# Kernel tuning notes

Hardware: AMD Instinct MI355X
Metric: run time of the kernel (lower is better)

Reference implementation:

```python
import jax, jax.numpy as jnp
import numpy as np

B, C_IN, C_OUT, N, K = 4, 64, 64, 100000, 6
EPS = 1e-5  # BatchNorm2d default eps


def setup_inputs() -> dict:
    key = jax.random.key(0)
    k1, k2, k3, k4 = jax.random.split(key, 4)
    x = jax.random.normal(k1, (B, C_IN, N), jnp.float32)
    neigh = jax.random.randint(k2, (B, N, K), 0, N, jnp.int32)
    # bias-free 1x2 conv weights (center feature + neighbor-sum symmetric operator)
    W0 = jax.random.normal(k3, (C_OUT, C_IN, 2), jnp.float32) * (1.0 / np.sqrt(C_IN * 2))
    W1 = jax.random.normal(k4, (C_OUT, C_OUT, 2), jnp.float32) * (1.0 / np.sqrt(C_OUT * 2))
    gamma = jnp.ones((C_OUT,), jnp.float32)
    beta = jnp.zeros((C_OUT,), jnp.float32)
    return {"x": x, "neigh": neigh, "W0": W0, "W1": W1, "gamma": gamma, "beta": beta}


def _mesh_conv_point(x, neigh, W):
    # x: [B, C, N], neigh: [B, N, K] -> gather neighbor features [B, C, N, K]
    nb = jax.vmap(lambda xb, ib: xb[:, ib])(x, neigh)
    # symmetric operator stack: center feature and sum over neighbors -> [B, C, N, 2]
    G = jnp.stack([x, nb.sum(axis=-1)], axis=-1)
    # 1x2 conv (bias=False) as einsum -> [B, O, N]
    return jnp.einsum('bcns,ocs->bon', G, W)


def _batchnorm(h, gamma, beta):
    # training-mode batch stats over (batch, vertex) per channel
    mean = h.mean(axis=(0, 2), keepdims=True)
    var = h.var(axis=(0, 2), keepdims=True)
    return (h - mean) * jax.lax.rsqrt(var + EPS) * gamma[None, :, None] + beta[None, :, None]


def reference(x, neigh, W0, W1, gamma, beta):
    h = _mesh_conv_point(x, neigh, W0)
    x1 = h  # residual branch
    h = _batchnorm(jax.nn.relu(h), gamma, beta)
    h = _mesh_conv_point(h, neigh, W1)
    h = h + x1
    return jax.nn.relu(h)
```

## Files before the change

kernel.cpp:

```cpp
#include <hip/hip_runtime.h>
#include <hip/hip_bf16.h>

#define BB   4
#define NN   100000
#define TOT  (BB * NN)
#define KK   6
#define EPSV 1e-5f

using bf16   = __hip_bfloat16;
using ushort = unsigned short;
typedef __attribute__((ext_vector_type(8))) short  short8;
typedef __attribute__((ext_vector_type(4))) float  float4v;

union U4S8 { uint4 u; short8 s; };

__device__ __forceinline__ unsigned f2bu(float f) {
    union { bf16 h; ushort u; } c; c.h = __float2bfloat16(f); return c.u;
}
__device__ __forceinline__ unsigned pk(float a, float b) {
    return f2bu(a) | (f2bu(b) << 16);
}
__device__ __forceinline__ float blo(unsigned x) {
    union { unsigned u; float f; } c; c.u = x << 16; return c.f;
}
__device__ __forceinline__ float bhi(unsigned x) {
    union { unsigned u; float f; } c; c.u = x & 0xFFFF0000u; return c.f;
}
__device__ __forceinline__ unsigned relu2(unsigned x) {
    unsigned lo = (unsigned)(((int)(x << 16)) >> 31) & 0x0000FFFFu;
    unsigned hi = ((unsigned)(((int)x) >> 31)) << 16;
    return x & ~(lo | hi);
}
__device__ __forceinline__ int batch_base(int g) {
    return (g >= 3 * NN) ? 3 * NN : (g >= 2 * NN) ? 2 * NN : (g >= NN) ? NN : 0;
}

__device__ __forceinline__ void gload_lds16(const void* g, void* l)
{
    __builtin_amdgcn_global_load_lds(
        (const __attribute__((address_space(1))) unsigned int*)g,
        (__attribute__((address_space(3))) unsigned int*)l, 16, 0, 0);
}

__global__ void wprep0_k(const float* __restrict__ W0, ushort* __restrict__ Wf0)
{
    int L = blockIdx.x * 256 + threadIdx.x;
    if (L < 8192) {
        int i = L & 7, lane = (L >> 3) & 63, r = L >> 9;
        int s = r & 1, t = r >> 1;
        int o = (t & 3) * 16 + (lane & 15);
        int c = s * 32 + (lane >> 4) * 8 + i;
        Wf0[L] = f2bu(W0[o * 128 + c * 2 + (t >> 2)]);
    }
}

__global__ __launch_bounds__(256) void xpose_k(const float* __restrict__ x,
                                               ushort* __restrict__ xT)
{
    __shared__ float tile[64][65];
    const int b  = blockIdx.y;
    const int n0 = blockIdx.x * 64;
    const int tx = threadIdx.x & 63;
    const int ty = threadIdx.x >> 6;
    const float* xb = x + (size_t)b * 64 * NN;
    const int n = n0 + tx;
#pragma unroll
    for (int cc = 0; cc < 64; cc += 4) {
        const int c = cc + ty;
        tile[tx][c] = (n < NN) ? xb[(size_t)c * NN + n] : 0.f;
    }
    __syncthreads();
#pragma unroll
    for (int rr = 0; rr < 64; rr += 4) {
        const int nl = rr + ty;
        const int n2 = n0 + nl;
        if (n2 < NN) xT[((size_t)b * NN + n2) * 64 + tx] = (ushort)f2bu(tile[nl][tx]);
    }
}

__global__ __launch_bounds__(256, 3) void gemm1_k(
    const ushort* __restrict__ xT, const ushort* __restrict__ Wf,
    ushort* __restrict__ Uu, ushort* __restrict__ Uv)
{
    const int wave = threadIdx.x >> 6;
    const int lane = threadIdx.x & 63;
    const int col  = lane & 15;
    const int quad = lane >> 4;

    short8 wf[8][2];
#pragma unroll
    for (int t = 0; t < 8; ++t)
#pragma unroll
        for (int s = 0; s < 2; ++s)
            wf[t][s] = *(const short8*)(Wf + ((t * 2 + s) * 64 + lane) * 8);

    const int wid = blockIdx.x * 4 + wave;
    for (int tile = wid; tile < 25000; tile += 2500) {
        const size_t g0 = (size_t)tile * 16;
        const ushort* ar = xT + (g0 + col) * 64 + quad * 8;
        short8 p0 = *(const short8*)(ar);
        short8 p1 = *(const short8*)(ar + 32);

        float4v acc[8];
#pragma unroll
        for (int t = 0; t < 8; ++t) acc[t] = (float4v){0.f, 0.f, 0.f, 0.f};
#pragma unroll
        for (int t = 0; t < 8; ++t)
            acc[t] = __builtin_amdgcn_mfma_f32_16x16x32_bf16(wf[t][0], p0, acc[t], 0, 0, 0);
#pragma unroll
        for (int t = 0; t < 8; ++t)
            acc[t] = __builtin_amdgcn_mfma_f32_16x16x32_bf16(wf[t][1], p1, acc[t], 0, 0, 0);

#pragma unroll
        for (int t = 0; t < 8; ++t) {
            uint2 d;
            d.x = pk(acc[t][0], acc[t][1]);
            d.y = pk(acc[t][2], acc[t][3]);
            ushort* base = (t < 4) ? Uu : Uv;
            *(uint2*)(base + (g0 + col) * 64 + (t & 3) * 16 + quad * 4) = d;
        }
    }
}

__global__ __launch_bounds__(256, 3) void gather1_k(
    const ushort* __restrict__ Uu, const ushort* __restrict__ Uv,
    const int* __restrict__ neigh, ushort* __restrict__ hT,
    float* __restrict__ stats)
{
    __shared__ __align__(1024) ushort stage[4][3072];
    __shared__ float red[4][128];
    const int wave = threadIdx.x >> 6;
    const int lane = threadIdx.x & 63;
    const int p    = lane >> 3;
    const int s    = lane & 7;
    const int g0   = (blockIdx.x * 4 + wave) * 32;

    ushort* stg = stage[wave];
    const int csw = ((s - p) & 7) * 8;
    const int rsw = ((s + p) & 7) * 8;
    const uint2* nbp = (const uint2*)neigh;

    float sA[8] = {0,0,0,0,0,0,0,0}, sB[8] = {0,0,0,0,0,0,0,0};

    for (int t = 0; t < 4; ++t) {
        const int gme = g0 + t * 8 + p;
        const int bo  = batch_base(gme);

        uint2 i01 = nbp[(size_t)gme * 3 + 0];
        uint2 i23 = nbp[(size_t)gme * 3 + 1];
        uint2 i45 = nbp[(size_t)gme * 3 + 2];
        int idx[6] = {(int)i01.x, (int)i01.y, (int)i23.x,
                      (int)i23.y, (int)i45.x, (int)i45.y};

        uint4 cu = *(const uint4*)(Uu + (size_t)gme * 64 + s * 8);

#pragma unroll
        for (int m = 0; m < 6; ++m)
            gload_lds16(Uv + (size_t)(bo + idx[m]) * 64 + csw, stg + m * 512);

        asm volatile("s_waitcnt vmcnt(0)" ::: "memory");

        float h[8];
        h[0] = blo(cu.x); h[1] = bhi(cu.x); h[2] = blo(cu.y); h[3] = bhi(cu.y);
        h[4] = blo(cu.z); h[5] = bhi(cu.z); h[6] = blo(cu.w); h[7] = bhi(cu.w);
#pragma unroll
        for (int m = 0; m < 6; ++m) {
            const uint4 r = *(const uint4*)(stg + m * 512 + p * 64 + rsw);
            h[0] += blo(r.x); h[1] += bhi(r.x); h[2] += blo(r.y); h[3] += bhi(r.y);
            h[4] += blo(r.z); h[5] += bhi(r.z); h[6] += blo(r.w); h[7] += bhi(r.w);
        }
        uint4 st;
        st.x = pk(h[0], h[1]); st.y = pk(h[2], h[3]);
        st.z = pk(h[4], h[5]); st.w = pk(h[6], h[7]);
        *(uint4*)(hT + (size_t)gme * 64 + s * 8) = st;
#pragma unroll
        for (int j = 0; j < 8; ++j) {
            float rv = fmaxf(h[j], 0.f);
            sA[j] += rv;
            sB[j]  = fmaf(rv, rv, sB[j]);
        }
    }

#pragma unroll
    for (int d = 8; d < 64; d <<= 1)
#pragma unroll
        for (int j = 0; j < 8; ++j) {
            sA[j] += __shfl_xor(sA[j], d);
            sB[j] += __shfl_xor(sB[j], d);
        }
    if (lane < 8) {
#pragma unroll
        for (int j = 0; j < 8; ++j) {
            red[wave][lane * 8 + j]      = sA[j];
            red[wave][64 + lane * 8 + j] = sB[j];
        }
    }
    __syncthreads();
    if (threadIdx.x < 128) {
        float v = red[0][threadIdx.x] + red[1][threadIdx.x]
                + red[2][threadIdx.x] + red[3][threadIdx.x];
        atomicAdd(&stats[threadIdx.x], v);
    }
}

__global__ void bnA_k(const float* __restrict__ stats, const float* __restrict__ gamma,
                      const float* __restrict__ beta, float* __restrict__ ab)
{
    const int o = threadIdx.x;
    if (o < 64) {
        const float inv = 1.f / (float)TOT;
        float mean = stats[o] * inv;
        float var  = stats[64 + o] * inv - mean * mean;
        float a    = gamma[o] * rsqrtf(var + EPSV);
        ab[o]      = a;
        ab[64 + o] = fmaf(-a, mean, beta[o]);
    }
}

__global__ __launch_bounds__(256) void bnB_k(
    const float* __restrict__ ab, const float* __restrict__ W1,
    ushort* __restrict__ Wf1, float* __restrict__ bias)
{
    if (blockIdx.x < 32) {
        int L = blockIdx.x * 256 + threadIdx.x;
        int i = L & 7, lane = (L >> 3) & 63, r = L >> 9;
        int s = r & 1, t = r >> 1;
        int o = (t & 3) * 16 + (lane & 15);
        int c = s * 32 + (lane >> 4) * 8 + i;
        Wf1[L] = f2bu(ab[c] * W1[o * 128 + c * 2 + (t >> 2)]);
    } else if (threadIdx.x < 128) {
        const int part = threadIdx.x >> 6, o = threadIdx.x & 63;
        float s = 0.f;
#pragma unroll
        for (int c = 0; c < 64; ++c)
            s = fmaf(ab[64 + c], W1[o * 128 + c * 2 + part], s);
        bias[threadIdx.x] = s;
    }
}

__global__ __launch_bounds__(256, 3) void gemm2_k(
    const ushort* __restrict__ hT, const ushort* __restrict__ Wf,
    const float* __restrict__ bias, ushort* __restrict__ Up,
    ushort* __restrict__ Uq)
{
    const int wave = threadIdx.x >> 6;
    const int lane = threadIdx.x & 63;
    const int col  = lane & 15;
    const int quad = lane >> 4;

    short8 wf[8][2];
#pragma unroll
    for (int t = 0; t < 8; ++t)
#pragma unroll
        for (int s = 0; s < 2; ++s)
            wf[t][s] = *(const short8*)(Wf + ((t * 2 + s) * 64 + lane) * 8);

    float4v binit[8];
#pragma unroll
    for (int t = 0; t < 8; ++t)
#pragma unroll
        for (int r = 0; r < 4; ++r)
            binit[t][r] = bias[t * 16 + quad * 4 + r];

    const int wid = blockIdx.x * 4 + wave;
    for (int tile = wid; tile < 25000; tile += 2500) {
        const size_t g0 = (size_t)tile * 16;
        const ushort* ar = hT + (g0 + col) * 64 + quad * 8;
        U4S8 p0, p1;
        p0.u = *(const uint4*)(ar);
        p1.u = *(const uint4*)(ar + 32);
        p0.u.x = relu2(p0.u.x); p0.u.y = relu2(p0.u.y);
        p0.u.z = relu2(p0.u.z); p0.u.w = relu2(p0.u.w);
        p1.u.x = relu2(p1.u.x); p1.u.y = relu2(p1.u.y);
        p1.u.z = relu2(p1.u.z); p1.u.w = relu2(p1.u.w);

        float4v acc[8];
#pragma unroll
        for (int t = 0; t < 8; ++t) acc[t] = binit[t];
#pragma unroll
        for (int t = 0; t < 8; ++t)
            acc[t] = __builtin_amdgcn_mfma_f32_16x16x32_bf16(wf[t][0], p0.s, acc[t], 0, 0, 0);
#pragma unroll
        for (int t = 0; t < 8; ++t)
            acc[t] = __builtin_amdgcn_mfma_f32_16x16x32_bf16(wf[t][1], p1.s, acc[t], 0, 0, 0);

#pragma unroll
        for (int t = 0; t < 8; ++t) {
            uint2 d;
            d.x = pk(acc[t][0], acc[t][1]);
            d.y = pk(acc[t][2], acc[t][3]);
            ushort* base = (t < 4) ? Up : Uq;
            *(uint2*)(base + (g0 + col) * 64 + (t & 3) * 16 + quad * 4) = d;
        }
    }
}

__global__ __launch_bounds__(256, 3) void gather2_k(
    const ushort* __restrict__ Up, const ushort* __restrict__ Uq,
    const ushort* __restrict__ hT, const int* __restrict__ neigh,
    float* __restrict__ out)
{
    __shared__ __align__(1024) ushort stage[4][3072];
    __shared__ float ts[64][65];
    const int wave = threadIdx.x >> 6;
    const int lane = threadIdx.x & 63;
    const int p    = lane >> 3;
    const int s    = lane & 7;
    const int g0   = blockIdx.x * 64;
    const int gw   = g0 + wave * 16;

    ushort* stg = stage[wave];
    const int csw = ((s - p) & 7) * 8;
    const int rsw = ((s + p) & 7) * 8;
    const uint2* nbp = (const uint2*)neigh;

#pragma unroll
    for (int t = 0; t < 2; ++t) {
        const int gme = gw + t * 8 + p;
        const int bo  = batch_base(gme);

        uint2 i01 = nbp[(size_t)gme * 3 + 0];
        uint2 i23 = nbp[(size_t)gme * 3 + 1];
        uint2 i45 = nbp[(size_t)gme * 3 + 2];
        int idx[6] = {(int)i01.x, (int)i01.y, (int)i23.x,
                      (int)i23.y, (int)i45.x, (int)i45.y};

        uint4 cp = *(const uint4*)(Up + (size_t)gme * 64 + s * 8);
        uint4 cr = *(const uint4*)(hT + (size_t)gme * 64 + s * 8);

#pragma unroll
        for (int m = 0; m < 6; ++m)
            gload_lds16(Uq + (size_t)(bo + idx[m]) * 64 + csw, stg + m * 512);

        asm volatile("s_waitcnt vmcnt(0)" ::: "memory");

        float h[8];
        h[0] = blo(cp.x) + blo(cr.x); h[1] = bhi(cp.x) + bhi(cr.x);
        h[2] = blo(cp.y) + blo(cr.y); h[3] = bhi(cp.y) + bhi(cr.y);
        h[4] = blo(cp.z) + blo(cr.z); h[5] = bhi(cp.z) + bhi(cr.z);
        h[6] = blo(cp.w) + blo(cr.w); h[7] = bhi(cp.w) + bhi(cr.w);
#pragma unroll
        for (int m = 0; m < 6; ++m) {
            const uint4 r = *(const uint4*)(stg + m * 512 + p * 64 + rsw);
            h[0] += blo(r.x); h[1] += bhi(r.x); h[2] += blo(r.y); h[3] += bhi(r.y);
            h[4] += blo(r.z); h[5] += bhi(r.z); h[6] += blo(r.w); h[7] += bhi(r.w);
        }
        const int pl = wave * 16 + t * 8 + p;
#pragma unroll
        for (int j = 0; j < 8; ++j)
            ts[s * 8 + j][pl] = fmaxf(h[j], 0.f);
    }
    __syncthreads();

    const int g2  = g0 + lane;
    const int bo2 = batch_base(g2);
    const int b2  = (g2 >= 3 * NN) ? 3 : (g2 >= 2 * NN) ? 2 : (g2 >= NN) ? 1 : 0;
    const int n2  = g2 - bo2;
#pragma unroll
    for (int r = 0; r < 16; ++r) {
        const int o = wave * 16 + r;
        out[((size_t)b2 * 64 + o) * NN + n2] = ts[o][lane];
    }
}

extern "C" void kernel_launch(void* const* d_in, const int* in_sizes, int n_in,
                              void* d_out, int out_size, void* d_ws, size_t ws_size,
                              hipStream_t stream)
{
    const float* x     = (const float*)d_in[0];
    const int*   neigh = (const int*)d_in[1];
    const float* W0    = (const float*)d_in[2];
    const float* W1    = (const float*)d_in[3];
    const float* gamma = (const float*)d_in[4];
    const float* beta  = (const float*)d_in[5];
    float* out = (float*)d_out;

    char* ws = (char*)d_ws;
    ushort* xT    = (ushort*)(ws + 0);
    ushort* hT    = (ushort*)(ws + 0);
    ushort* Uu    = (ushort*)(ws + 51200000);
    ushort* Uv    = (ushort*)(ws + 102400000);
    ushort* Up    = Uu;
    ushort* Uq    = Uv;
    float*  stats = (float*)(ws + 153600000);
    float*  ab    = (float*)(ws + 153600512);
    ushort* Wf0   = (ushort*)(ws + 153601024);
    ushort* Wf1   = (ushort*)(ws + 153617408);
    float*  bias  = (float*)(ws + 153633792);

    hipMemsetAsync(stats, 0, 512, stream);
    wprep0_k<<<dim3(32), dim3(256), 0, stream>>>(W0, Wf0);
    xpose_k<<<dim3((NN + 63) / 64, BB), dim3(256), 0, stream>>>(x, xT);
    gemm1_k<<<dim3(625), dim3(256), 0, stream>>>(xT, Wf0, Uu, Uv);
    gather1_k<<<dim3(3125), dim3(256), 0, stream>>>(Uu, Uv, neigh, hT, stats);
    bnA_k<<<dim3(1), dim3(64), 0, stream>>>(stats, gamma, beta, ab);
    bnB_k<<<dim3(33), dim3(256), 0, stream>>>(ab, W1, Wf1, bias);
    gemm2_k<<<dim3(625), dim3(256), 0, stream>>>(hT, Wf1, bias, Up, Uq);
    gather2_k<<<dim3(TOT / 64), dim3(256), 0, stream>>>(Up, Uq, hT, neigh, out);
}
```

Baseline: 442.9 us.

## Split channel-major intermediates into 16-channel planes for cache-friendly neighbor gathers

Intermediate bf16 tensors are stored as four 16-channel planes of size TOT*16 instead of 64 contiguous channels per vertex. Each gather wave then handles a single plane, so the random neighbor reads for a pass touch a 12.8MB working set that may fit better in cache. The LDS staging via global_load_lds is replaced with direct uint4 register loads, and grids grow to 12500 blocks with higher occupancy bounds. The trade-off is that neighbor indices are reloaded four times, and each gathered row is now a smaller 32-byte segment.

```diff
diff --git a/kernel.cpp b/kernel.cpp
--- a/kernel.cpp
+++ b/kernel.cpp
@@ -31,16 +31,8 @@
     unsigned hi = ((unsigned)(((int)x) >> 31)) << 16;
     return x & ~(lo | hi);
 }
-__device__ __forceinline__ int batch_base(int g) {
-    return (g >= 3 * NN) ? 3 * NN : (g >= 2 * NN) ? 2 * NN : (g >= NN) ? NN : 0;
-}
-
-__device__ __forceinline__ void gload_lds16(const void* g, void* l)
-{
-    __builtin_amdgcn_global_load_lds(
-        (const __attribute__((address_space(1))) unsigned int*)g,
-        (__attribute__((address_space(3))) unsigned int*)l, 16, 0, 0);
-}
+
+#define PST ((size_t)TOT * 16)
 
 __global__ void wprep0_k(const float* __restrict__ W0, ushort* __restrict__ Wf0)
 {
@@ -117,89 +109,84 @@
             d.x = pk(acc[t][0], acc[t][1]);
             d.y = pk(acc[t][2], acc[t][3]);
             ushort* base = (t < 4) ? Uu : Uv;
-            *(uint2*)(base + (g0 + col) * 64 + (t & 3) * 16 + quad * 4) = d;
+            *(uint2*)(base + ((size_t)(t & 3) * TOT + g0 + col) * 16 + quad * 4) = d;
         }
     }
 }
 
-__global__ __launch_bounds__(256, 3) void gather1_k(
+__global__ __launch_bounds__(256, 6) void gather1_k(
     const ushort* __restrict__ Uu, const ushort* __restrict__ Uv,
     const int* __restrict__ neigh, ushort* __restrict__ hT,
     float* __restrict__ stats)
 {
-    __shared__ __align__(1024) ushort stage[4][3072];
-    __shared__ float red[4][128];
+    __shared__ float red[4][32];
     const int wave = threadIdx.x >> 6;
     const int lane = threadIdx.x & 63;
-    const int p    = lane >> 3;
-    const int s    = lane & 7;
-    const int g0   = (blockIdx.x * 4 + wave) * 32;
-
-    ushort* stg = stage[wave];
-    const int csw = ((s - p) & 7) * 8;
-    const int rsw = ((s + p) & 7) * 8;
-    const uint2* nbp = (const uint2*)neigh;
-
-    float sA[8] = {0,0,0,0,0,0,0,0}, sB[8] = {0,0,0,0,0,0,0,0};
-
-    for (int t = 0; t < 4; ++t) {
-        const int gme = g0 + t * 8 + p;
-        const int bo  = batch_base(gme);
-
-        uint2 i01 = nbp[(size_t)gme * 3 + 0];
-        uint2 i23 = nbp[(size_t)gme * 3 + 1];
-        uint2 i45 = nbp[(size_t)gme * 3 + 2];
-        int idx[6] = {(int)i01.x, (int)i01.y, (int)i23.x,
-                      (int)i23.y, (int)i45.x, (int)i45.y};
-
-        uint4 cu = *(const uint4*)(Uu + (size_t)gme * 64 + s * 8);
-
-#pragma unroll
-        for (int m = 0; m < 6; ++m)
-            gload_lds16(Uv + (size_t)(bo + idx[m]) * 64 + csw, stg + m * 512);
-
-        asm volatile("s_waitcnt vmcnt(0)" ::: "memory");
-
-        float h[8];
-        h[0] = blo(cu.x); h[1] = bhi(cu.x); h[2] = blo(cu.y); h[3] = bhi(cu.y);
-        h[4] = blo(cu.z); h[5] = bhi(cu.z); h[6] = blo(cu.w); h[7] = bhi(cu.w);
-#pragma unroll
-        for (int m = 0; m < 6; ++m) {
-            const uint4 r = *(const uint4*)(stg + m * 512 + p * 64 + rsw);
-            h[0] += blo(r.x); h[1] += bhi(r.x); h[2] += blo(r.y); h[3] += bhi(r.y);
-            h[4] += blo(r.z); h[5] += bhi(r.z); h[6] += blo(r.w); h[7] += bhi(r.w);
-        }
-        uint4 st;
-        st.x = pk(h[0], h[1]); st.y = pk(h[2], h[3]);
-        st.z = pk(h[4], h[5]); st.w = pk(h[6], h[7]);
-        *(uint4*)(hT + (size_t)gme * 64 + s * 8) = st;
-#pragma unroll
-        for (int j = 0; j < 8; ++j) {
-            float rv = fmaxf(h[j], 0.f);
-            sA[j] += rv;
-            sB[j]  = fmaf(rv, rv, sB[j]);
-        }
-    }
-
-#pragma unroll
-    for (int d = 8; d < 64; d <<= 1)
+    const int p    = lane >> 1;
+    const int e    = lane & 1;
+    const int wid  = blockIdx.x * 4 + wave;
+    const int q    = wid / 12500;
+    const int r    = wid - q * 12500;
+    const int b    = r / 3125;
+    const int grp  = r - b * 3125;
+    const int gme  = b * NN + grp * 32 + p;
+    const int bo   = b * NN;
+    const int eo   = e * 8;
+
+    const int* np = neigh + (size_t)gme * 6;
+    const uint2 i01 = *(const uint2*)(np);
+    const uint2 i23 = *(const uint2*)(np + 2);
+    const uint2 i45 = *(const uint2*)(np + 4);
+
+    const ushort* uvb = Uv + q * PST;
+    uint4 v0 = *(const uint4*)(uvb + ((size_t)(bo + (int)i01.x)) * 16 + eo);
+    uint4 v1 = *(const uint4*)(uvb + ((size_t)(bo + (int)i01.y)) * 16 + eo);
+    uint4 v2 = *(const uint4*)(uvb + ((size_t)(bo + (int)i23.x)) * 16 + eo);
+    uint4 v3 = *(const uint4*)(uvb + ((size_t)(bo + (int)i23.y)) * 16 + eo);
+    uint4 v4 = *(const uint4*)(uvb + ((size_t)(bo + (int)i45.x)) * 16 + eo);
+    uint4 v5 = *(const uint4*)(uvb + ((size_t)(bo + (int)i45.y)) * 16 + eo);
+    uint4 cu = *(const uint4*)(Uu + q * PST + (size_t)gme * 16 + eo);
+
+    float h[8];
+    h[0] = blo(cu.x); h[1] = bhi(cu.x); h[2] = blo(cu.y); h[3] = bhi(cu.y);
+    h[4] = blo(cu.z); h[5] = bhi(cu.z); h[6] = blo(cu.w); h[7] = bhi(cu.w);
+#define ACC8(v) { h[0]+=blo(v.x); h[1]+=bhi(v.x); h[2]+=blo(v.y); h[3]+=bhi(v.y); \
+                  h[4]+=blo(v.z); h[5]+=bhi(v.z); h[6]+=blo(v.w); h[7]+=bhi(v.w); }
+    ACC8(v0) ACC8(v1) ACC8(v2) ACC8(v3) ACC8(v4) ACC8(v5)
+
+    uint4 st;
+    st.x = pk(h[0], h[1]); st.y = pk(h[2], h[3]);
+    st.z = pk(h[4], h[5]); st.w = pk(h[6], h[7]);
+    *(uint4*)(hT + q * PST + (size_t)gme * 16 + eo) = st;
+
+    float sA[8], sB[8];
+#pragma unroll
+    for (int j = 0; j < 8; ++j) {
+        float rv = fmaxf(h[j], 0.f);
+        sA[j] = rv;
+        sB[j] = rv * rv;
+    }
+#pragma unroll
+    for (int d = 2; d < 64; d <<= 1)
 #pragma unroll
         for (int j = 0; j < 8; ++j) {
             sA[j] += __shfl_xor(sA[j], d);
             sB[j] += __shfl_xor(sB[j], d);
         }
-    if (lane < 8) {
+    if (lane < 2) {
 #pragma unroll
         for (int j = 0; j < 8; ++j) {
             red[wave][lane * 8 + j]      = sA[j];
-            red[wave][64 + lane * 8 + j] = sB[j];
+            red[wave][16 + lane * 8 + j] = sB[j];
         }
     }
     __syncthreads();
-    if (threadIdx.x < 128) {
+    if (threadIdx.x < 32) {
+        const int q0 = blockIdx.x / 3125;
         float v = red[0][threadIdx.x] + red[1][threadIdx.x]
                 + red[2][threadIdx.x] + red[3][threadIdx.x];
-        atomicAdd(&stats[threadIdx.x], v);
+        const int c = threadIdx.x & 15;
+        atomicAdd(&stats[(threadIdx.x < 16 ? 0 : 64) + q0 * 16 + c], v);
     }
 }
 
@@ -265,10 +252,10 @@
     const int wid = blockIdx.x * 4 + wave;
     for (int tile = wid; tile < 25000; tile += 2500) {
         const size_t g0 = (size_t)tile * 16;
-        const ushort* ar = hT + (g0 + col) * 64 + quad * 8;
+        const ushort* ar = hT + ((size_t)(quad >> 1) * TOT + g0 + col) * 16 + (quad & 1) * 8;
         U4S8 p0, p1;
         p0.u = *(const uint4*)(ar);
-        p1.u = *(const uint4*)(ar + 32);
+        p1.u = *(const uint4*)(ar + 2 * PST);
         p0.u.x = relu2(p0.u.x); p0.u.y = relu2(p0.u.y);
         p0.u.z = relu2(p0.u.z); p0.u.w = relu2(p0.u.w);
         p1.u.x = relu2(p1.u.x); p1.u.y = relu2(p1.u.y);
@@ -290,77 +277,55 @@
             d.x = pk(acc[t][0], acc[t][1]);
             d.y = pk(acc[t][2], acc[t][3]);
             ushort* base = (t < 4) ? Up : Uq;
-            *(uint2*)(base + (g0 + col) * 64 + (t & 3) * 16 + quad * 4) = d;
+            *(uint2*)(base + ((size_t)(t & 3) * TOT + g0 + col) * 16 + quad * 4) = d;
         }
     }
 }
 
-__global__ __launch_bounds__(256, 3) void gather2_k(
+__global__ __launch_bounds__(256, 6) void gather2_k(
     const ushort* __restrict__ Up, const ushort* __restrict__ Uq,
     const ushort* __restrict__ hT, const int* __restrict__ neigh,
     float* __restrict__ out)
 {
-    __shared__ __align__(1024) ushort stage[4][3072];
-    __shared__ float ts[64][65];
     const int wave = threadIdx.x >> 6;
     const int lane = threadIdx.x & 63;
-    const int p    = lane >> 3;
-    const int s    = lane & 7;
-    const int g0   = blockIdx.x * 64;
-    const int gw   = g0 + wave * 16;
-
-    ushort* stg = stage[wave];
-    const int csw = ((s - p) & 7) * 8;
-    const int rsw = ((s + p) & 7) * 8;
-    const uint2* nbp = (const uint2*)neigh;
-
-#pragma unroll
-    for (int t = 0; t < 2; ++t) {
-        const int gme = gw + t * 8 + p;
-        const int bo  = batch_base(gme);
-
-        uint2 i01 = nbp[(size_t)gme * 3 + 0];
-        uint2 i23 = nbp[(size_t)gme * 3 + 1];
-        uint2 i45 = nbp[(size_t)gme * 3 + 2];
-        int idx[6] = {(int)i01.x, (int)i01.y, (int)i23.x,
-                      (int)i23.y, (int)i45.x, (int)i45.y};
-
-        uint4 cp = *(const uint4*)(Up + (size_t)gme * 64 + s * 8);
-        uint4 cr = *(const uint4*)(hT + (size_t)gme * 64 + s * 8);
-
-#pragma unroll
-        for (int m = 0; m < 6; ++m)
-            gload_lds16(Uq + (size_t)(bo + idx[m]) * 64 + csw, stg + m * 512);
-
-        asm volatile("s_waitcnt vmcnt(0)" ::: "memory");
-
-        float h[8];
-        h[0] = blo(cp.x) + blo(cr.x); h[1] = bhi(cp.x) + bhi(cr.x);
-        h[2] = blo(cp.y) + blo(cr.y); h[3] = bhi(cp.y) + bhi(cr.y);
-        h[4] = blo(cp.z) + blo(cr.z); h[5] = bhi(cp.z) + bhi(cr.z);
-        h[6] = blo(cp.w) + blo(cr.w); h[7] = bhi(cp.w) + bhi(cr.w);
-#pragma unroll
-        for (int m = 0; m < 6; ++m) {
-            const uint4 r = *(const uint4*)(stg + m * 512 + p * 64 + rsw);
-            h[0] += blo(r.x); h[1] += bhi(r.x); h[2] += blo(r.y); h[3] += bhi(r.y);
-            h[4] += blo(r.z); h[5] += bhi(r.z); h[6] += blo(r.w); h[7] += bhi(r.w);
-        }
-        const int pl = wave * 16 + t * 8 + p;
-#pragma unroll
-        for (int j = 0; j < 8; ++j)
-            ts[s * 8 + j][pl] = fmaxf(h[j], 0.f);
-    }
-    __syncthreads();
-
-    const int g2  = g0 + lane;
-    const int bo2 = batch_base(g2);
-    const int b2  = (g2 >= 3 * NN) ? 3 : (g2 >= 2 * NN) ? 2 : (g2 >= NN) ? 1 : 0;
-    const int n2  = g2 - bo2;
-#pragma unroll
-    for (int r = 0; r < 16; ++r) {
-        const int o = wave * 16 + r;
-        out[((size_t)b2 * 64 + o) * NN + n2] = ts[o][lane];
-    }
+    const int p    = lane >> 1;
+    const int e    = lane & 1;
+    const int wid  = blockIdx.x * 4 + wave;
+    const int q    = wid / 12500;
+    const int r    = wid - q * 12500;
+    const int b    = r / 3125;
+    const int grp  = r - b * 3125;
+    const int gme  = b * NN + grp * 32 + p;
+    const int bo   = b * NN;
+    const int eo   = e * 8;
+
+    const int* np = neigh + (size_t)gme * 6;
+    const uint2 i01 = *(const uint2*)(np);
+    const uint2 i23 = *(const uint2*)(np + 2);
+    const uint2 i45 = *(const uint2*)(np + 4);
+
+    const ushort* uqb = Uq + q * PST;
+    uint4 v0 = *(const uint4*)(uqb + ((size_t)(bo + (int)i01.x)) * 16 + eo);
+    uint4 v1 = *(const uint4*)(uqb + ((size_t)(bo + (int)i01.y)) * 16 + eo);
+    uint4 v2 = *(const uint4*)(uqb + ((size_t)(bo + (int)i23.x)) * 16 + eo);
+    uint4 v3 = *(const uint4*)(uqb + ((size_t)(bo + (int)i23.y)) * 16 + eo);
+    uint4 v4 = *(const uint4*)(uqb + ((size_t)(bo + (int)i45.x)) * 16 + eo);
+    uint4 v5 = *(const uint4*)(uqb + ((size_t)(bo + (int)i45.y)) * 16 + eo);
+    uint4 cp = *(const uint4*)(Up + q * PST + (size_t)gme * 16 + eo);
+    uint4 cr = *(const uint4*)(hT + q * PST + (size_t)gme * 16 + eo);
+
+    float h[8];
+    h[0] = blo(cp.x) + blo(cr.x); h[1] = bhi(cp.x) + bhi(cr.x);
+    h[2] = blo(cp.y) + blo(cr.y); h[3] = bhi(cp.y) + bhi(cr.y);
+    h[4] = blo(cp.z) + blo(cr.z); h[5] = bhi(cp.z) + bhi(cr.z);
+    h[6] = blo(cp.w) + blo(cr.w); h[7] = bhi(cp.w) + bhi(cr.w);
+    ACC8(v0) ACC8(v1) ACC8(v2) ACC8(v3) ACC8(v4) ACC8(v5)
+
+    float* ob = out + ((size_t)(b * 64 + q * 16 + e * 8)) * NN + grp * 32 + p;
+#pragma unroll
+    for (int j = 0; j < 8; ++j)
+        ob[(size_t)j * NN] = fmaxf(h[j], 0.f);
 }
 
 extern "C" void kernel_launch(void* const* d_in, const int* in_sizes, int n_in,
@@ -392,9 +357,9 @@
     wprep0_k<<<dim3(32), dim3(256), 0, stream>>>(W0, Wf0);
     xpose_k<<<dim3((NN + 63) / 64, BB), dim3(256), 0, stream>>>(x, xT);
     gemm1_k<<<dim3(625), dim3(256), 0, stream>>>(xT, Wf0, Uu, Uv);
-    gather1_k<<<dim3(3125), dim3(256), 0, stream>>>(Uu, Uv, neigh, hT, stats);
+    gather1_k<<<dim3(12500), dim3(256), 0, stream>>>(Uu, Uv, neigh, hT, stats);
     bnA_k<<<dim3(1), dim3(64), 0, stream>>>(stats, gamma, beta, ab);
     bnB_k<<<dim3(33), dim3(256), 0, stream>>>(ab, W1, Wf1, bias);
     gemm2_k<<<dim3(625), dim3(256), 0, stream>>>(hT, Wf1, bias, Up, Uq);
-    gather2_k<<<dim3(TOT / 64), dim3(256), 0, stream>>>(Up, Uq, hT, neigh, out);
-}
+    gather2_k<<<dim3(12500), dim3(256), 0, stream>>>(Up, Uq, hT, neigh, out);
+}
```

After: 476.5 us. 7.6% more time.

## Gather neighbor features before the GEMM and fuse the output transpose into gemm2

Applied to the files above, without the earlier changes.

Each mesh-conv stage now sums the 64-channel input features over the neighbors first (gatherx/gatherh), then runs a single K=128 MFMA GEMM over [center, neighbor-sum]. Before, the GEMM produced two 64-channel projections and the neighbor gather ran on the projected outputs. The reordering is meant to cut intermediate global-memory traffic: one sum buffer replaces the two projected buffers. BN statistics move into gemm1, and BN's shift is folded into the bias as 6x the neighbor weight. gemm2 now adds the residual and applies ReLU, then transposes through shared memory straight to the output, which removes the separate gather2 pass and its LDS-staged async loads. The risk is the extra gather passes, whose random 16-byte loads now go through plain vector loads.

```diff
diff --git a/kernel.cpp b/kernel.cpp
--- a/kernel.cpp
+++ b/kernel.cpp
@@ -35,22 +35,21 @@
     return (g >= 3 * NN) ? 3 * NN : (g >= 2 * NN) ? 2 * NN : (g >= NN) ? NN : 0;
 }
 
-__device__ __forceinline__ void gload_lds16(const void* g, void* l)
-{
-    __builtin_amdgcn_global_load_lds(
-        (const __attribute__((address_space(1))) unsigned int*)g,
-        (__attribute__((address_space(3))) unsigned int*)l, 16, 0, 0);
-}
+#define ACC8(v)  { h[0]+=blo(v.x); h[1]+=bhi(v.x); h[2]+=blo(v.y); h[3]+=bhi(v.y); \
+                   h[4]+=blo(v.z); h[5]+=bhi(v.z); h[6]+=blo(v.w); h[7]+=bhi(v.w); }
+#define ACCR8(v) { unsigned a0=relu2(v.x),a1=relu2(v.y),a2=relu2(v.z),a3=relu2(v.w); \
+                   h[0]+=blo(a0); h[1]+=bhi(a0); h[2]+=blo(a1); h[3]+=bhi(a1); \
+                   h[4]+=blo(a2); h[5]+=bhi(a2); h[6]+=blo(a3); h[7]+=bhi(a3); }
 
 __global__ void wprep0_k(const float* __restrict__ W0, ushort* __restrict__ Wf0)
 {
     int L = blockIdx.x * 256 + threadIdx.x;
     if (L < 8192) {
         int i = L & 7, lane = (L >> 3) & 63, r = L >> 9;
-        int s = r & 1, t = r >> 1;
-        int o = (t & 3) * 16 + (lane & 15);
-        int c = s * 32 + (lane >> 4) * 8 + i;
-        Wf0[L] = f2bu(W0[o * 128 + c * 2 + (t >> 2)]);
+        int t = r >> 2, ks = r & 3;
+        int o = t * 16 + (lane & 15);
+        int c = ks * 32 + (lane >> 4) * 8 + i;
+        Wf0[L] = f2bu(W0[o * 128 + (c & 63) * 2 + (c >> 6)]);
     }
 }
 
@@ -78,122 +77,122 @@
     }
 }
 
+__global__ __launch_bounds__(256, 4) void gatherx_k(
+    const ushort* __restrict__ xT, const int* __restrict__ neigh,
+    ushort* __restrict__ SX)
+{
+    const int wave = threadIdx.x >> 6;
+    const int lane = threadIdx.x & 63;
+    const int p    = lane >> 3;
+    const int s    = lane & 7;
+    const int so   = s * 8;
+    const int g0   = (blockIdx.x * 4 + wave) * 32;
+
+#pragma unroll
+    for (int t = 0; t < 4; ++t) {
+        const int gme = g0 + t * 8 + p;
+        const int bo  = batch_base(gme);
+        const int* np = neigh + (size_t)gme * 6;
+        const uint2 i01 = *(const uint2*)(np);
+        const uint2 i23 = *(const uint2*)(np + 2);
+        const uint2 i45 = *(const uint2*)(np + 4);
+
+        uint4 v0 = *(const uint4*)(xT + (size_t)(bo + (int)i01.x) * 64 + so);
+        uint4 v1 = *(const uint4*)(xT + (size_t)(bo + (int)i01.y) * 64 + so);
+        uint4 v2 = *(const uint4*)(xT + (size_t)(bo + (int)i23.x) * 64 + so);
+        uint4 v3 = *(const uint4*)(xT + (size_t)(bo + (int)i23.y) * 64 + so);
+        uint4 v4 = *(const uint4*)(xT + (size_t)(bo + (int)i45.x) * 64 + so);
+        uint4 v5 = *(const uint4*)(xT + (size_t)(bo + (int)i45.y) * 64 + so);
+
+        float h[8] = {0, 0, 0, 0, 0, 0, 0, 0};
+        ACC8(v0) ACC8(v1) ACC8(v2) ACC8(v3) ACC8(v4) ACC8(v5)
+
+        uint4 st;
+        st.x = pk(h[0], h[1]); st.y = pk(h[2], h[3]);
+        st.z = pk(h[4], h[5]); st.w = pk(h[6], h[7]);
+        *(uint4*)(SX + (size_t)gme * 64 + so) = st;
+    }
+}
+
 __global__ __launch_bounds__(256, 3) void gemm1_k(
-    const ushort* __restrict__ xT, const ushort* __restrict__ Wf,
-    ushort* __restrict__ Uu, ushort* __restrict__ Uv)
-{
+    const ushort* __restrict__ xT, const ushort* __restrict__ SX,
+    const ushort* __restrict__ Wf, ushort* __restrict__ hT,
+    float* __restrict__ stats)
+{
+    __shared__ float red[4][128];
     const int wave = threadIdx.x >> 6;
     const int lane = threadIdx.x & 63;
     const int col  = lane & 15;
     const int quad = lane >> 4;
 
-    short8 wf[8][2];
-#pragma unroll
-    for (int t = 0; t < 8; ++t)
-#pragma unroll
-        for (int s = 0; s < 2; ++s)
-            wf[t][s] = *(const short8*)(Wf + ((t * 2 + s) * 64 + lane) * 8);
+    short8 wf[4][4];
+#pragma unroll
+    for (int t = 0; t < 4; ++t)
+#pragma unroll
+        for (int ks = 0; ks < 4; ++ks)
+            wf[t][ks] = *(const short8*)(Wf + ((t * 4 + ks) * 64 + lane) * 8);
+
+    float sA[16], sB[16];
+#pragma unroll
+    for (int j = 0; j < 16; ++j) { sA[j] = 0.f; sB[j] = 0.f; }
 
     const int wid = blockIdx.x * 4 + wave;
     for (int tile = wid; tile < 25000; tile += 2500) {
         const size_t g0 = (size_t)tile * 16;
-        const ushort* ar = xT + (g0 + col) * 64 + quad * 8;
-        short8 p0 = *(const short8*)(ar);
-        short8 p1 = *(const short8*)(ar + 32);
-
-        float4v acc[8];
-#pragma unroll
-        for (int t = 0; t < 8; ++t) acc[t] = (float4v){0.f, 0.f, 0.f, 0.f};
-#pragma unroll
-        for (int t = 0; t < 8; ++t)
+        const ushort* xr = xT + (g0 + col) * 64 + quad * 8;
+        const ushort* sr = SX + (g0 + col) * 64 + quad * 8;
+        short8 p0 = *(const short8*)(xr);
+        short8 p1 = *(const short8*)(xr + 32);
+        short8 p2 = *(const short8*)(sr);
+        short8 p3 = *(const short8*)(sr + 32);
+
+        float4v acc[4];
+#pragma unroll
+        for (int t = 0; t < 4; ++t) acc[t] = (float4v){0.f, 0.f, 0.f, 0.f};
+#pragma unroll
+        for (int t = 0; t < 4; ++t)
             acc[t] = __builtin_amdgcn_mfma_f32_16x16x32_bf16(wf[t][0], p0, acc[t], 0, 0, 0);
 #pragma unroll
-        for (int t = 0; t < 8; ++t)
+        for (int t = 0; t < 4; ++t)
             acc[t] = __builtin_amdgcn_mfma_f32_16x16x32_bf16(wf[t][1], p1, acc[t], 0, 0, 0);
-
-#pragma unroll
-        for (int t = 0; t < 8; ++t) {
+#pragma unroll
+        for (int t = 0; t < 4; ++t)
+            acc[t] = __builtin_amdgcn_mfma_f32_16x16x32_bf16(wf[t][2], p2, acc[t], 0, 0, 0);
+#pragma unroll
+        for (int t = 0; t < 4; ++t)
+            acc[t] = __builtin_amdgcn_mfma_f32_16x16x32_bf16(wf[t][3], p3, acc[t], 0, 0, 0);
+
+#pragma unroll
+        for (int t = 0; t < 4; ++t) {
             uint2 d;
             d.x = pk(acc[t][0], acc[t][1]);
             d.y = pk(acc[t][2], acc[t][3]);
-            ushort* base = (t < 4) ? Uu : Uv;
-            *(uint2*)(base + (g0 + col) * 64 + (t & 3) * 16 + quad * 4) = d;
+            *(uint2*)(hT + (g0 + col) * 64 + t * 16 + quad * 4) = d;
+#pragma unroll
+            for (int r = 0; r < 4; ++r) {
+                float rv = fmaxf(acc[t][r], 0.f);
+                sA[t * 4 + r] += rv;
+                sB[t * 4 + r]  = fmaf(rv, rv, sB[t * 4 + r]);
+            }
         }
     }
-}
-
-__global__ __launch_bounds__(256, 3) void gather1_k(
-    const ushort* __restrict__ Uu, const ushort* __restrict__ Uv,
-    const int* __restrict__ neigh, ushort* __restrict__ hT,
-    float* __restrict__ stats)
-{
-    __shared__ __align__(1024) ushort stage[4][3072];
-    __shared__ float red[4][128];
-    const int wave = threadIdx.x >> 6;
-    const int lane = threadIdx.x & 63;
-    const int p    = lane >> 3;
-    const int s    = lane & 7;
-    const int g0   = (blockIdx.x * 4 + wave) * 32;
-
-    ushort* stg = stage[wave];
-    const int csw = ((s - p) & 7) * 8;
-    const int rsw = ((s + p) & 7) * 8;
-    const uint2* nbp = (const uint2*)neigh;
-
-    float sA[8] = {0,0,0,0,0,0,0,0}, sB[8] = {0,0,0,0,0,0,0,0};
-
-    for (int t = 0; t < 4; ++t) {
-        const int gme = g0 + t * 8 + p;
-        const int bo  = batch_base(gme);
-
-        uint2 i01 = nbp[(size_t)gme * 3 + 0];
-        uint2 i23 = nbp[(size_t)gme * 3 + 1];
-        uint2 i45 = nbp[(size_t)gme * 3 + 2];
-        int idx[6] = {(int)i01.x, (int)i01.y, (int)i23.x,
-                      (int)i23.y, (int)i45.x, (int)i45.y};
-
-        uint4 cu = *(const uint4*)(Uu + (size_t)gme * 64 + s * 8);
-
-#pragma unroll
-        for (int m = 0; m < 6; ++m)
-            gload_lds16(Uv + (size_t)(bo + idx[m]) * 64 + csw, stg + m * 512);
-
-        asm volatile("s_waitcnt vmcnt(0)" ::: "memory");
-
-        float h[8];
-        h[0] = blo(cu.x); h[1] = bhi(cu.x); h[2] = blo(cu.y); h[3] = bhi(cu.y);
-        h[4] = blo(cu.z); h[5] = bhi(cu.z); h[6] = blo(cu.w); h[7] = bhi(cu.w);
-#pragma unroll
-        for (int m = 0; m < 6; ++m) {
-            const uint4 r = *(const uint4*)(stg + m * 512 + p * 64 + rsw);
-            h[0] += blo(r.x); h[1] += bhi(r.x); h[2] += blo(r.y); h[3] += bhi(r.y);
-            h[4] += blo(r.z); h[5] += bhi(r.z); h[6] += blo(r.w); h[7] += bhi(r.w);
-        }
-        uint4 st;
-        st.x = pk(h[0], h[1]); st.y = pk(h[2], h[3]);
-        st.z = pk(h[4], h[5]); st.w = pk(h[6], h[7]);
-        *(uint4*)(hT + (size_t)gme * 64 + s * 8) = st;
-#pragma unroll
-        for (int j = 0; j < 8; ++j) {
-            float rv = fmaxf(h[j], 0.f);
-            sA[j] += rv;
-            sB[j]  = fmaf(rv, rv, sB[j]);
-        }
-    }
-
-#pragma unroll
-    for (int d = 8; d < 64; d <<= 1)
-#pragma unroll
-        for (int j = 0; j < 8; ++j) {
+
+#pragma unroll
+    for (int d = 1; d < 16; d <<= 1)
+#pragma unroll
+        for (int j = 0; j < 16; ++j) {
             sA[j] += __shfl_xor(sA[j], d);
             sB[j] += __shfl_xor(sB[j], d);
         }
-    if (lane < 8) {
-#pragma unroll
-        for (int j = 0; j < 8; ++j) {
-            red[wave][lane * 8 + j]      = sA[j];
-            red[wave][64 + lane * 8 + j] = sB[j];
-        }
+    if (col == 0) {
+#pragma unroll
+        for (int t = 0; t < 4; ++t)
+#pragma unroll
+            for (int r = 0; r < 4; ++r) {
+                const int o = t * 16 + quad * 4 + r;
+                red[wave][o]      = sA[t * 4 + r];
+                red[wave][64 + o] = sB[t * 4 + r];
+            }
     }
     __syncthreads();
     if (threadIdx.x < 128) {
@@ -224,142 +223,138 @@
     if (blockIdx.x < 32) {
         int L = blockIdx.x * 256 + threadIdx.x;
         int i = L & 7, lane = (L >> 3) & 63, r = L >> 9;
-        int s = r & 1, t = r >> 1;
-        int o = (t & 3) * 16 + (lane & 15);
-        int c = s * 32 + (lane >> 4) * 8 + i;
-        Wf1[L] = f2bu(ab[c] * W1[o * 128 + c * 2 + (t >> 2)]);
-    } else if (threadIdx.x < 128) {
-        const int part = threadIdx.x >> 6, o = threadIdx.x & 63;
+        int t = r >> 2, ks = r & 3;
+        int o = t * 16 + (lane & 15);
+        int c = ks * 32 + (lane >> 4) * 8 + i;
+        int cc = c & 63;
+        Wf1[L] = f2bu(ab[cc] * W1[o * 128 + cc * 2 + (c >> 6)]);
+    } else if (threadIdx.x < 64) {
+        const int o = threadIdx.x;
         float s = 0.f;
 #pragma unroll
         for (int c = 0; c < 64; ++c)
-            s = fmaf(ab[64 + c], W1[o * 128 + c * 2 + part], s);
-        bias[threadIdx.x] = s;
+            s += ab[64 + c] * (W1[o * 128 + c * 2] + 6.f * W1[o * 128 + c * 2 + 1]);
+        bias[o] = s;
+    }
+}
+
+__global__ __launch_bounds__(256, 4) void gatherh_k(
+    const ushort* __restrict__ hT, const int* __restrict__ neigh,
+    ushort* __restrict__ SH)
+{
+    const int wave = threadIdx.x >> 6;
+    const int lane = threadIdx.x & 63;
+    const int p    = lane >> 3;
+    const int s    = lane & 7;
+    const int so   = s * 8;
+    const int g0   = (blockIdx.x * 4 + wave) * 32;
+
+#pragma unroll
+    for (int t = 0; t < 4; ++t) {
+        const int gme = g0 + t * 8 + p;
+        const int bo  = batch_base(gme);
+        const int* np = neigh + (size_t)gme * 6;
+        const uint2 i01 = *(const uint2*)(np);
+        const uint2 i23 = *(const uint2*)(np + 2);
+        const uint2 i45 = *(const uint2*)(np + 4);
+
+        uint4 v0 = *(const uint4*)(hT + (size_t)(bo + (int)i01.x) * 64 + so);
+        uint4 v1 = *(const uint4*)(hT + (size_t)(bo + (int)i01.y) * 64 + so);
+        uint4 v2 = *(const uint4*)(hT + (size_t)(bo + (int)i23.x) * 64 + so);
+        uint4 v3 = *(const uint4*)(hT + (size_t)(bo + (int)i23.y) * 64 + so);
+        uint4 v4 = *(const uint4*)(hT + (size_t)(bo + (int)i45.x) * 64 + so);
+        uint4 v5 = *(const uint4*)(hT + (size_t)(bo + (int)i45.y) * 64 + so);
+
+        float h[8] = {0, 0, 0, 0, 0, 0, 0, 0};
+        ACCR8(v0) ACCR8(v1) ACCR8(v2) ACCR8(v3) ACCR8(v4) ACCR8(v5)
+
+        uint4 st;
+        st.x = pk(h[0], h[1]); st.y = pk(h[2], h[3]);
+        st.z = pk(h[4], h[5]); st.w = pk(h[6], h[7]);
+        *(uint4*)(SH + (size_t)gme * 64 + so) = st;
     }
 }
 
 __global__ __launch_bounds__(256, 3) void gemm2_k(
-    const ushort* __restrict__ hT, const ushort* __restrict__ Wf,
-    const float* __restrict__ bias, ushort* __restrict__ Up,
-    ushort* __restrict__ Uq)
-{
+    const ushort* __restrict__ hT, const ushort* __restrict__ SH,
+    const ushort* __restrict__ Wf, const float* __restrict__ bias,
+    float* __restrict__ out)
+{
+    __shared__ float ts[64][65];
     const int wave = threadIdx.x >> 6;
     const int lane = threadIdx.x & 63;
     const int col  = lane & 15;
     const int quad = lane >> 4;
 
-    short8 wf[8][2];
-#pragma unroll
-    for (int t = 0; t < 8; ++t)
-#pragma unroll
-        for (int s = 0; s < 2; ++s)
-            wf[t][s] = *(const short8*)(Wf + ((t * 2 + s) * 64 + lane) * 8);
-
-    float4v binit[8];
-#pragma unroll
-    for (int t = 0; t < 8; ++t)
+    short8 wf[4][4];
+#pragma unroll
+    for (int t = 0; t < 4; ++t)
+#pragma unroll
+        for (int ks = 0; ks < 4; ++ks)
+            wf[t][ks] = *(const short8*)(Wf + ((t * 4 + ks) * 64 + lane) * 8);
+
+    float binit[16];
+#pragma unroll
+    for (int t = 0; t < 4; ++t)
 #pragma unroll
         for (int r = 0; r < 4; ++r)
-            binit[t][r] = bias[t * 16 + quad * 4 + r];
-
-    const int wid = blockIdx.x * 4 + wave;
-    for (int tile = wid; tile < 25000; tile += 2500) {
-        const size_t g0 = (size_t)tile * 16;
-        const ushort* ar = hT + (g0 + col) * 64 + quad * 8;
-        U4S8 p0, p1;
-        p0.u = *(const uint4*)(ar);
-        p1.u = *(const uint4*)(ar + 32);
+            binit[t * 4 + r] = bias[t * 16 + quad * 4 + r];
+
+    for (int it = 0; it < 10; ++it) {
+        const int gb = (blockIdx.x * 10 + it) * 64;
+        const size_t g0 = (size_t)gb + wave * 16;
+        const ushort* hr = hT + (g0 + col) * 64 + quad * 8;
+        const ushort* sr = SH + (g0 + col) * 64 + quad * 8;
+        U4S8 p0, p1, p2, p3;
+        p0.u = *(const uint4*)(hr);
+        p1.u = *(const uint4*)(hr + 32);
+        p2.u = *(const uint4*)(sr);
+        p3.u = *(const uint4*)(sr + 32);
         p0.u.x = relu2(p0.u.x); p0.u.y = relu2(p0.u.y);
         p0.u.z = relu2(p0.u.z); p0.u.w = relu2(p0.u.w);
         p1.u.x = relu2(p1.u.x); p1.u.y = relu2(p1.u.y);
         p1.u.z = relu2(p1.u.z); p1.u.w = relu2(p1.u.w);
 
-        float4v acc[8];
-#pragma unroll
-        for (int t = 0; t < 8; ++t) acc[t] = binit[t];
-#pragma unroll
-        for (int t = 0; t < 8; ++t)
+        float4v acc[4];
+#pragma unroll
+        for (int t = 0; t < 4; ++t)
+            acc[t] = (float4v){binit[t * 4], binit[t * 4 + 1],
+                               binit[t * 4 + 2], binit[t * 4 + 3]};
+#pragma unroll
+        for (int t = 0; t < 4; ++t)
             acc[t] = __builtin_amdgcn_mfma_f32_16x16x32_bf16(wf[t][0], p0.s, acc[t], 0, 0, 0);
 #pragma unroll
-        for (int t = 0; t < 8; ++t)
+        for (int t = 0; t < 4; ++t)
             acc[t] = __builtin_amdgcn_mfma_f32_16x16x32_bf16(wf[t][1], p1.s, acc[t], 0, 0, 0);
-
-#pragma unroll
-        for (int t = 0; t < 8; ++t) {
-            uint2 d;
-            d.x = pk(acc[t][0], acc[t][1]);
-            d.y = pk(acc[t][2], acc[t][3]);
-            ushort* base = (t < 4) ? Up : Uq;
-            *(uint2*)(base + (g0 + col) * 64 + (t & 3) * 16 + quad * 4) = d;
+#pragma unroll
+        for (int t = 0; t < 4; ++t)
+            acc[t] = __builtin_amdgcn_mfma_f32_16x16x32_bf16(wf[t][2], p2.s, acc[t], 0, 0, 0);
+#pragma unroll
+        for (int t = 0; t < 4; ++t)
+            acc[t] = __builtin_amdgcn_mfma_f32_16x16x32_bf16(wf[t][3], p3.s, acc[t], 0, 0, 0);
+
+        const int pl = wave * 16 + col;
+#pragma unroll
+        for (int t = 0; t < 4; ++t) {
+            const uint2 rd = *(const uint2*)(hT + (g0 + col) * 64 + t * 16 + quad * 4);
+            const int o = t * 16 + quad * 4;
+            ts[o + 0][pl] = fmaxf(acc[t][0] + blo(rd.x), 0.f);
+            ts[o + 1][pl] = fmaxf(acc[t][1] + bhi(rd.x), 0.f);
+            ts[o + 2][pl] = fmaxf(acc[t][2] + blo(rd.y), 0.f);
+            ts[o + 3][pl] = fmaxf(acc[t][3] + bhi(rd.y), 0.f);
         }
-    }
-}
-
-__global__ __launch_bounds__(256, 3) void gather2_k(
-    const ushort* __restrict__ Up, const ushort* __restrict__ Uq,
-    const ushort* __restrict__ hT, const int* __restrict__ neigh,
-    float* __restrict__ out)
-{
-    __shared__ __align__(1024) ushort stage[4][3072];
-    __shared__ float ts[64][65];
-    const int wave = threadIdx.x >> 6;
-    const int lane = threadIdx.x & 63;
-    const int p    = lane >> 3;
-    const int s    = lane & 7;
-    const int g0   = blockIdx.x * 64;
-    const int gw   = g0 + wave * 16;
-
-    ushort* stg = stage[wave];
-    const int csw = ((s - p) & 7) * 8;
-    const int rsw = ((s + p) & 7) * 8;
-    const uint2* nbp = (const uint2*)neigh;
-
-#pragma unroll
-    for (int t = 0; t < 2; ++t) {
-        const int gme = gw + t * 8 + p;
-        const int bo  = batch_base(gme);
-
-        uint2 i01 = nbp[(size_t)gme * 3 + 0];
-        uint2 i23 = nbp[(size_t)gme * 3 + 1];
-        uint2 i45 = nbp[(size_t)gme * 3 + 2];
-        int idx[6] = {(int)i01.x, (int)i01.y, (int)i23.x,
-                      (int)i23.y, (int)i45.x, (int)i45.y};
-
-        uint4 cp = *(const uint4*)(Up + (size_t)gme * 64 + s * 8);
-        uint4 cr = *(const uint4*)(hT + (size_t)gme * 64 + s * 8);
-
-#pragma unroll
-        for (int m = 0; m < 6; ++m)
-            gload_lds16(Uq + (size_t)(bo + idx[m]) * 64 + csw, stg + m * 512);
-
-        asm volatile("s_waitcnt vmcnt(0)" ::: "memory");
-
-        float h[8];
-        h[0] = blo(cp.x) + blo(cr.x); h[1] = bhi(cp.x) + bhi(cr.x);
-        h[2] = blo(cp.y) + blo(cr.y); h[3] = bhi(cp.y) + bhi(cr.y);
-        h[4] = blo(cp.z) + blo(cr.z); h[5] = bhi(cp.z) + bhi(cr.z);
-        h[6] = blo(cp.w) + blo(cr.w); h[7] = bhi(cp.w) + bhi(cr.w);
-#pragma unroll
-        for (int m = 0; m < 6; ++m) {
-            const uint4 r = *(const uint4*)(stg + m * 512 + p * 64 + rsw);
-            h[0] += blo(r.x); h[1] += bhi(r.x); h[2] += blo(r.y); h[3] += bhi(r.y);
-            h[4] += blo(r.z); h[5] += bhi(r.z); h[6] += blo(r.w); h[7] += bhi(r.w);
+        __syncthreads();
+
+        const int g2  = gb + lane;
+        const int bo2 = batch_base(g2);
+        const int b2  = (g2 >= 3 * NN) ? 3 : (g2 >= 2 * NN) ? 2 : (g2 >= NN) ? 1 : 0;
+        const int n2  = g2 - bo2;
+#pragma unroll
+        for (int r = 0; r < 16; ++r) {
+            const int o = wave * 16 + r;
+            out[((size_t)b2 * 64 + o) * NN + n2] = ts[o][lane];
         }
-        const int pl = wave * 16 + t * 8 + p;
-#pragma unroll
-        for (int j = 0; j < 8; ++j)
-            ts[s * 8 + j][pl] = fmaxf(h[j], 0.f);
-    }
-    __syncthreads();
-
-    const int g2  = g0 + lane;
-    const int bo2 = batch_base(g2);
-    const int b2  = (g2 >= 3 * NN) ? 3 : (g2 >= 2 * NN) ? 2 : (g2 >= NN) ? 1 : 0;
-    const int n2  = g2 - bo2;
-#pragma unroll
-    for (int r = 0; r < 16; ++r) {
-        const int o = wave * 16 + r;
-        out[((size_t)b2 * 64 + o) * NN + n2] = ts[o][lane];
+        __syncthreads();
     }
 }
 
@@ -377,11 +372,9 @@
 
     char* ws = (char*)d_ws;
     ushort* xT    = (ushort*)(ws + 0);
-    ushort* hT    = (ushort*)(ws + 0);
-    ushort* Uu    = (ushort*)(ws + 51200000);
-    ushort* Uv    = (ushort*)(ws + 102400000);
-    ushort* Up    = Uu;
-    ushort* Uq    = Uv;
+    ushort* SX    = (ushort*)(ws + 51200000);
+    ushort* SH    = SX;
+    ushort* hT    = (ushort*)(ws + 102400000);
     float*  stats = (float*)(ws + 153600000);
     float*  ab    = (float*)(ws + 153600512);
     ushort* Wf0   = (ushort*)(ws + 153601024);
@@ -391,10 +384,10 @@
     hipMemsetAsync(stats, 0, 512, stream);
     wprep0_k<<<dim3(32), dim3(256), 0, stream>>>(W0, Wf0);
     xpose_k<<<dim3((NN + 63) / 64, BB), dim3(256), 0, stream>>>(x, xT);
-    gemm1_k<<<dim3(625), dim3(256), 0, stream>>>(xT, Wf0, Uu, Uv);
-    gather1_k<<<dim3(3125), dim3(256), 0, stream>>>(Uu, Uv, neigh, hT, stats);
+    gatherx_k<<<dim3(3125), dim3(256), 0, stream>>>(xT, neigh, SX);
+    gemm1_k<<<dim3(625), dim3(256), 0, stream>>>(xT, SX, Wf0, hT, stats);
     bnA_k<<<dim3(1), dim3(64), 0, stream>>>(stats, gamma, beta, ab);
     bnB_k<<<dim3(33), dim3(256), 0, stream>>>(ab, W1, Wf1, bias);
-    gemm2_k<<<dim3(625), dim3(256), 0, stream>>>(hT, Wf1, bias, Up, Uq);
-    gather2_k<<<dim3(TOT / 64), dim3(256), 0, stream>>>(Up, Uq, hT, neigh, out);
-}
+    gatherh_k<<<dim3(3125), dim3(256), 0, stream>>>(hT, neigh, SH);
+    gemm2_k<<<dim3(625), dim3(256), 0, stream>>>(hT, SH, Wf1, bias, out);
+}
```

Result: faster. 370.2 us (-16.4%).
